# Performance work log

Hardware: AMD Instinct MI355X
Metric: run time of the kernel (lower is better)

The kernel has to match this reference:

```python
import jax, jax.numpy as jnp
import numpy as np

HIDDEN = 1024
INTER = 4096
NUM_EXPERTS = 8
TOP_K = 2


def setup_inputs() -> dict:
    key = jax.random.key(0)
    k1, k2, k3, k4 = jax.random.split(key, 4)
    hidden_states = jax.random.normal(k1, (4, 1024, HIDDEN), dtype=jnp.float32)
    gate_w = jax.random.normal(k2, (HIDDEN, NUM_EXPERTS), dtype=jnp.float32) * 0.02
    w1 = jax.random.normal(k3, (NUM_EXPERTS, HIDDEN, INTER), dtype=jnp.float32) * 0.02
    w2 = jax.random.normal(k4, (NUM_EXPERTS, INTER, HIDDEN), dtype=jnp.float32) * 0.02
    return {"hidden_states": hidden_states, "gate_w": gate_w, "w1": w1, "w2": w2}


def reference(hidden_states, gate_w, w1, w2):
    B, S, H = hidden_states.shape
    x = hidden_states.reshape(-1, H)                       # [T, H]
    T = x.shape[0]
    router_logits = x @ gate_w                             # [T, E]
    probs = jax.nn.softmax(router_logits.astype(jnp.float32), axis=-1)
    routing_weights, selected_experts = jax.lax.top_k(probs, TOP_K)  # [T, K]
    routing_weights = routing_weights / routing_weights.sum(-1, keepdims=True)
    routing_weights = routing_weights.astype(x.dtype)
    # combine[t, e] = sum_k rw[t, k] * (sel[t, k] == e)
    combine = jnp.zeros((T, NUM_EXPERTS), x.dtype).at[
        jnp.arange(T)[:, None], selected_experts
    ].add(routing_weights)
    # dense grouped MLP over all experts; zero combine weight drops unrouted pairs
    h1 = jax.nn.gelu(jnp.einsum('th,ehi->tei', x, w1), approximate=False)  # [T, E, I]
    y = jnp.einsum('tei,eih->teh', h1, w2)                 # [T, E, H]
    out = jnp.einsum('teh,te->th', y, combine)             # [T, H]
    return out.reshape(B, S, H), router_logits
```

## Files before the change

### kernel.cpp

```cpp
#include <hip/hip_runtime.h>
#include <hip/hip_bf16.h>
#include <math.h>

typedef unsigned short u16;
typedef unsigned int u32;
typedef __bf16 bf16x8 __attribute__((ext_vector_type(8)));
typedef float f32x4 __attribute__((ext_vector_type(4)));

#define T_TOK 4096
#define HID   1024
#define INTER 4096
#define NEXP  8

#define WS_NEEDED 209978368ull

__device__ __forceinline__ u16 f2bf(float f) {
    u32 u = __builtin_bit_cast(u32, f);
    u += 0x7FFFu + ((u >> 16) & 1u);
    return (u16)(u >> 16);
}

__device__ __forceinline__ void gl2lds16(const void* g, void* l) {
    __builtin_amdgcn_global_load_lds(
        (const __attribute__((address_space(1))) u32*)g,
        (__attribute__((address_space(3))) u32*)l, 16, 0, 0);
}

__device__ __forceinline__ float fast_gelu(float v) {
    float u2 = v * (-1.5957691216f - 0.0713548163f * v * v);
    return v / (1.0f + __expf(u2));
}

__global__ __launch_bounds__(256) void router_kernel(
    const float* __restrict__ x, const float* __restrict__ gw,
    float* __restrict__ logits, int* __restrict__ counts,
    int* __restrict__ tlist, float* __restrict__ wlist)
{
    const int lane = threadIdx.x & 63, wv = threadIdx.x >> 6;
    const int t = blockIdx.x * 4 + wv;
    const float* xr = x + (size_t)t * HID;
    float a[8] = {0.f,0.f,0.f,0.f,0.f,0.f,0.f,0.f};
    for (int h = lane; h < HID; h += 64) {
        float xv = xr[h];
        const float4* g4 = (const float4*)(gw + h * 8);
        float4 g0 = g4[0], g1 = g4[1];
        a[0] += xv * g0.x; a[1] += xv * g0.y; a[2] += xv * g0.z; a[3] += xv * g0.w;
        a[4] += xv * g1.x; a[5] += xv * g1.y; a[6] += xv * g1.z; a[7] += xv * g1.w;
    }
#pragma unroll
    for (int e = 0; e < 8; e++) {
        float v = a[e];
        for (int o = 32; o > 0; o >>= 1) v += __shfl_down(v, o, 64);
        a[e] = v;
    }
    if (lane == 0) {
#pragma unroll
        for (int e = 0; e < 8; e++) logits[(size_t)t * 8 + e] = a[e];
        int e1 = 0; float b1 = a[0];
        for (int e = 1; e < 8; e++) if (a[e] > b1) { b1 = a[e]; e1 = e; }
        int e2 = -1; float b2 = -1e30f;
        for (int e = 0; e < 8; e++) if (e != e1 && a[e] > b2) { b2 = a[e]; e2 = e; }
        float wa = 1.0f / (1.0f + expf(b2 - b1));
        float wb = 1.0f - wa;
        int p = atomicAdd(&counts[e1], 1);
        tlist[e1 * T_TOK + p] = t; wlist[e1 * T_TOK + p] = wa;
        p = atomicAdd(&counts[e2], 1);
        tlist[e2 * T_TOK + p] = t; wlist[e2 * T_TOK + p] = wb;
    }
}

__global__ void scan_kernel(const int* __restrict__ counts, int* __restrict__ offs)
{
    if (threadIdx.x == 0) {
        int s = 0;
        for (int e = 0; e < 8; e++) { offs[e] = s; s += counts[e]; }
    }
}

__global__ __launch_bounds__(256) void convert_x_kernel(
    const float* __restrict__ src, u16* __restrict__ dst)
{
    const int idx = (blockIdx.x * 256 + threadIdx.x) * 8;
    float4 f0 = *(const float4*)(src + idx);
    float4 f1 = *(const float4*)(src + idx + 4);
    uint4 o;
    o.x = (u32)f2bf(f0.x) | ((u32)f2bf(f0.y) << 16);
    o.y = (u32)f2bf(f0.z) | ((u32)f2bf(f0.w) << 16);
    o.z = (u32)f2bf(f1.x) | ((u32)f2bf(f1.y) << 16);
    o.w = (u32)f2bf(f1.z) | ((u32)f2bf(f1.w) << 16);
    *(uint4*)(dst + idx) = o;
}

__global__ __launch_bounds__(256) void transpose_convert_kernel(
    const float* __restrict__ src, u16* __restrict__ dst, int R, int C)
{
    __shared__ float tl[64][65];
    const int e = blockIdx.z;
    const int c0 = blockIdx.x * 64, r0 = blockIdx.y * 64;
    const float* s = src + (size_t)e * R * C + (size_t)r0 * C + c0;
    const int tid = threadIdx.x;
#pragma unroll
    for (int it = 0; it < 4; it++) {
        int idx = it * 256 + tid;
        int r = idx >> 4;
        int c4 = (idx & 15) * 4;
        float4 v = *(const float4*)(s + (size_t)r * C + c4);
        tl[c4 + 0][r] = v.x;
        tl[c4 + 1][r] = v.y;
        tl[c4 + 2][r] = v.z;
        tl[c4 + 3][r] = v.w;
    }
    __syncthreads();
    u16* d = dst + (size_t)e * C * R + (size_t)c0 * R + r0;
#pragma unroll
    for (int it = 0; it < 2; it++) {
        int idx = it * 256 + tid;
        int c = idx >> 3;
        int rg = (idx & 7) * 8;
        u32 o[4];
#pragma unroll
        for (int p = 0; p < 4; p++)
            o[p] = (u32)f2bf(tl[c][rg + 2 * p]) | ((u32)f2bf(tl[c][rg + 2 * p + 1]) << 16);
        *(uint4*)(d + (size_t)c * R + rg) = *(uint4*)o;
    }
}

__global__ __launch_bounds__(256, 1) void gemm1_kernel(
    const u16* __restrict__ xb, const u16* __restrict__ w1t,
    const int* __restrict__ counts, const int* __restrict__ offs,
    const int* __restrict__ tlist, u16* __restrict__ h1b)
{
    const int e = blockIdx.z, mt = blockIdx.y, nt = blockIdx.x;
    const int cnt = counts[e];
    if (mt * 128 >= cnt) return;
    __shared__ __align__(16) u16 As[8192];
    __shared__ __align__(16) u16 Bs[8192];
    __shared__ int toks[128];
    const int tid = threadIdx.x, lane = tid & 63, wv = tid >> 6;
    if (tid < 128) toks[tid] = tlist[e * T_TOK + min(mt * 128 + tid, cnt - 1)];
    __syncthreads();

    f32x4 acc[4][4] = {};
    const int wm = wv & 1, wn = wv >> 1;
    const int sj = tid >> 3, sp = tid & 7;

    size_t abase[4], bbase[4];
    const u16* w1base = w1t + ((size_t)e * INTER + (size_t)nt * 128) * HID;
#pragma unroll
    for (int j = 0; j < 4; j++) {
        int m = j * 32 + sj;
        abase[j] = (size_t)toks[m] * HID + ((sp - m) & 7) * 8;
        bbase[j] = (size_t)m * HID + ((sp - m) & 7) * 8;
    }

    for (int h0 = 0; h0 < HID; h0 += 64) {
#pragma unroll
        for (int j = 0; j < 4; j++)
            gl2lds16(xb + abase[j] + h0, &As[j * 2048 + wv * 512]);
#pragma unroll
        for (int j = 0; j < 4; j++)
            gl2lds16(w1base + bbase[j] + h0, &Bs[j * 2048 + wv * 512]);
        __syncthreads();
#pragma unroll
        for (int kk = 0; kk < 2; kk++) {
            bf16x8 a[4], b[4];
            const int jjb = kk * 4 + (lane >> 4);
#pragma unroll
            for (int i = 0; i < 4; i++) {
                int m = wm * 64 + i * 16 + (lane & 15);
                a[i] = *(const bf16x8*)&As[m * 64 + ((jjb + m) & 7) * 8];
            }
#pragma unroll
            for (int i = 0; i < 4; i++) {
                int n = wn * 64 + i * 16 + (lane & 15);
                b[i] = *(const bf16x8*)&Bs[n * 64 + ((jjb + n) & 7) * 8];
            }
#pragma unroll
            for (int i = 0; i < 4; i++)
#pragma unroll
                for (int j = 0; j < 4; j++)
                    acc[i][j] = __builtin_amdgcn_mfma_f32_16x16x32_bf16(
                        a[i], b[j], acc[i][j], 0, 0, 0);
        }
        __syncthreads();
    }

    const int pb = offs[e] + mt * 128;
    const bool full = (mt * 128 + 128 <= cnt);
#pragma unroll
    for (int i = 0; i < 4; i++) {
        const int mb = wm * 64 + i * 16 + ((lane >> 4) << 2);
#pragma unroll
        for (int j = 0; j < 4; j++) {
            const int n = nt * 128 + wn * 64 + j * 16 + (lane & 15);
#pragma unroll
            for (int r = 0; r < 4; r++) {
                const int m = mb + r;
                if (full || mt * 128 + m < cnt) {
                    h1b[(size_t)(pb + m) * INTER + n] = f2bf(fast_gelu(acc[i][j][r]));
                }
            }
        }
    }
}

__global__ __launch_bounds__(256, 1) void gemm2_kernel(
    const u16* __restrict__ h1b, const u16* __restrict__ w2t,
    const int* __restrict__ counts, const int* __restrict__ offs,
    const int* __restrict__ tlist, const float* __restrict__ wlist,
    float* __restrict__ out)
{
    const int e = blockIdx.z, mt = blockIdx.y;
    const int nt = blockIdx.x & 7, ks = blockIdx.x >> 3;
    const int cnt = counts[e];
    if (mt * 128 >= cnt) return;
    __shared__ __align__(16) u16 As[8192];
    __shared__ __align__(16) u16 Bs[8192];
    __shared__ int toks[128];
    __shared__ float wgt[128];
    const int tid = threadIdx.x, lane = tid & 63, wv = tid >> 6;
    if (tid < 128) {
        int gi = e * T_TOK + min(mt * 128 + tid, cnt - 1);
        toks[tid] = tlist[gi];
        wgt[tid] = wlist[gi];
    }
    __syncthreads();

    f32x4 acc[4][4] = {};
    const int wm = wv & 1, wn = wv >> 1;
    const int sj = tid >> 3, sp = tid & 7;

    size_t abase[4], bbase[4];
    const u16* w2base = w2t + ((size_t)e * HID + (size_t)nt * 128) * INTER;
    const int prow = offs[e];
#pragma unroll
    for (int j = 0; j < 4; j++) {
        int m = j * 32 + sj;
        int row = prow + min(mt * 128 + m, cnt - 1);
        abase[j] = (size_t)row * INTER + ((sp - m) & 7) * 8;
        bbase[j] = (size_t)m * INTER + ((sp - m) & 7) * 8;
    }

    const int i_lo = ks * (INTER / 2), i_hi = i_lo + (INTER / 2);
    for (int i0 = i_lo; i0 < i_hi; i0 += 64) {
#pragma unroll
        for (int j = 0; j < 4; j++)
            gl2lds16(h1b + abase[j] + i0, &As[j * 2048 + wv * 512]);
#pragma unroll
        for (int j = 0; j < 4; j++)
            gl2lds16(w2base + bbase[j] + i0, &Bs[j * 2048 + wv * 512]);
        __syncthreads();
#pragma unroll
        for (int kk = 0; kk < 2; kk++) {
            bf16x8 a[4], b[4];
            const int jjb = kk * 4 + (lane >> 4);
#pragma unroll
            for (int i = 0; i < 4; i++) {
                int m = wm * 64 + i * 16 + (lane & 15);
                a[i] = *(const bf16x8*)&As[m * 64 + ((jjb + m) & 7) * 8];
            }
#pragma unroll
            for (int i = 0; i < 4; i++) {
                int n = wn * 64 + i * 16 + (lane & 15);
                b[i] = *(const bf16x8*)&Bs[n * 64 + ((jjb + n) & 7) * 8];
            }
#pragma unroll
            for (int i = 0; i < 4; i++)
#pragma unroll
                for (int j = 0; j < 4; j++)
                    acc[i][j] = __builtin_amdgcn_mfma_f32_16x16x32_bf16(
                        a[i], b[j], acc[i][j], 0, 0, 0);
        }
        __syncthreads();
    }

    const bool full = (mt * 128 + 128 <= cnt);
#pragma unroll
    for (int i = 0; i < 4; i++) {
        const int mb = wm * 64 + i * 16 + ((lane >> 4) << 2);
#pragma unroll
        for (int j = 0; j < 4; j++) {
            const int n = nt * 128 + wn * 64 + j * 16 + (lane & 15);
#pragma unroll
            for (int r = 0; r < 4; r++) {
                const int m = mb + r;
                if (full || mt * 128 + m < cnt) {
                    atomicAdd(&out[(size_t)toks[m] * HID + n], acc[i][j][r] * wgt[m]);
                }
            }
        }
    }
}

extern "C" void kernel_launch(void* const* d_in, const int* in_sizes, int n_in,
                              void* d_out, int out_size, void* d_ws, size_t ws_size,
                              hipStream_t stream)
{
    const float* x  = (const float*)d_in[0];
    const float* gw = (const float*)d_in[1];
    const float* w1 = (const float*)d_in[2];
    const float* w2 = (const float*)d_in[3];
    float* out    = (float*)d_out;
    float* logits = out + 4194304;

    char* ws = (char*)d_ws;
    int*   counts = (int*)ws;
    int*   offs   = (int*)(ws + 256);
    int*   tlist  = (int*)(ws + 1024);
    float* wlist  = (float*)(ws + 132096);
    u16*   xb     = (u16*)(ws + 263168);
    u16*   w1t    = (u16*)(ws + 8651776);
    u16*   w2t    = (u16*)(ws + 75760640);
    u16*   h1b    = (u16*)(ws + 142869504);

    if (ws_size < WS_NEEDED) return;

    hipMemsetAsync(out, 0, 4194304 * sizeof(float), stream);
    hipMemsetAsync(counts, 0, 256, stream);

    router_kernel<<<1024, 256, 0, stream>>>(x, gw, logits, counts, tlist, wlist);
    scan_kernel<<<1, 64, 0, stream>>>(counts, offs);
    convert_x_kernel<<<2048, 256, 0, stream>>>(x, xb);
    transpose_convert_kernel<<<dim3(64, 16, 8), 256, 0, stream>>>(w1, w1t, HID, INTER);
    transpose_convert_kernel<<<dim3(16, 64, 8), 256, 0, stream>>>(w2, w2t, INTER, HID);

    gemm1_kernel<<<dim3(32, 16, 8), 256, 0, stream>>>(xb, w1t, counts, offs, tlist, h1b);
    gemm2_kernel<<<dim3(16, 16, 8), 256, 0, stream>>>(h1b, w2t, counts, offs, tlist, wlist, out);
}
```

Measured before the change: 707.5 us.

## Enlarge GEMM M-tile to 256, remap blocks per XCD, allow two blocks per CU

New measurement: 714.4 us. No clear change (+1.0%).

```diff
diff --git a/kernel.cpp b/kernel.cpp
--- a/kernel.cpp
+++ b/kernel.cpp
@@ -11,6 +11,10 @@
 #define HID   1024
 #define INTER 4096
 #define NEXP  8
+
+#define BM 256
+#define BN 128
+#define BK 64
 
 #define WS_NEEDED 209978368ull
 
@@ -125,37 +129,45 @@
     }
 }
 
-__global__ __launch_bounds__(256, 1) void gemm1_kernel(
+__global__ __launch_bounds__(256, 2) void gemm1_kernel(
     const u16* __restrict__ xb, const u16* __restrict__ w1t,
     const int* __restrict__ counts, const int* __restrict__ offs,
     const int* __restrict__ tlist, u16* __restrict__ h1b)
 {
-    const int e = blockIdx.z, mt = blockIdx.y, nt = blockIdx.x;
+    const int g = blockIdx.x & 7, p = blockIdx.x >> 3;
+    const int w = g * 256 + p;
+    const int e = w >> 8;
+    const int nt = (w >> 3) & 31;
+    const int mt = w & 7;
     const int cnt = counts[e];
-    if (mt * 128 >= cnt) return;
-    __shared__ __align__(16) u16 As[8192];
-    __shared__ __align__(16) u16 Bs[8192];
-    __shared__ int toks[128];
+    if (mt * BM >= cnt) return;
+    __shared__ __align__(16) u16 As[BM * BK];
+    __shared__ __align__(16) u16 Bs[BN * BK];
+    __shared__ int toks[BM];
     const int tid = threadIdx.x, lane = tid & 63, wv = tid >> 6;
-    if (tid < 128) toks[tid] = tlist[e * T_TOK + min(mt * 128 + tid, cnt - 1)];
+    toks[tid] = tlist[e * T_TOK + min(mt * BM + tid, cnt - 1)];
     __syncthreads();
 
-    f32x4 acc[4][4] = {};
+    f32x4 acc[8][4] = {};
     const int wm = wv & 1, wn = wv >> 1;
     const int sj = tid >> 3, sp = tid & 7;
 
-    size_t abase[4], bbase[4];
-    const u16* w1base = w1t + ((size_t)e * INTER + (size_t)nt * 128) * HID;
+    size_t abase[8], bbase[4];
+    const u16* w1base = w1t + ((size_t)e * INTER + (size_t)nt * BN) * HID;
+#pragma unroll
+    for (int j = 0; j < 8; j++) {
+        int m = j * 32 + sj;
+        abase[j] = (size_t)toks[m] * HID + ((sp - m) & 7) * 8;
+    }
 #pragma unroll
     for (int j = 0; j < 4; j++) {
         int m = j * 32 + sj;
-        abase[j] = (size_t)toks[m] * HID + ((sp - m) & 7) * 8;
         bbase[j] = (size_t)m * HID + ((sp - m) & 7) * 8;
     }
 
-    for (int h0 = 0; h0 < HID; h0 += 64) {
-#pragma unroll
-        for (int j = 0; j < 4; j++)
+    for (int h0 = 0; h0 < HID; h0 += BK) {
+#pragma unroll
+        for (int j = 0; j < 8; j++)
             gl2lds16(xb + abase[j] + h0, &As[j * 2048 + wv * 512]);
 #pragma unroll
         for (int j = 0; j < 4; j++)
@@ -163,20 +175,20 @@
         __syncthreads();
 #pragma unroll
         for (int kk = 0; kk < 2; kk++) {
-            bf16x8 a[4], b[4];
+            bf16x8 a[8], b[4];
             const int jjb = kk * 4 + (lane >> 4);
 #pragma unroll
-            for (int i = 0; i < 4; i++) {
-                int m = wm * 64 + i * 16 + (lane & 15);
+            for (int i = 0; i < 8; i++) {
+                int m = wm * 128 + i * 16 + (lane & 15);
                 a[i] = *(const bf16x8*)&As[m * 64 + ((jjb + m) & 7) * 8];
             }
 #pragma unroll
-            for (int i = 0; i < 4; i++) {
-                int n = wn * 64 + i * 16 + (lane & 15);
-                b[i] = *(const bf16x8*)&Bs[n * 64 + ((jjb + n) & 7) * 8];
-            }
-#pragma unroll
-            for (int i = 0; i < 4; i++)
+            for (int j = 0; j < 4; j++) {
+                int n = wn * 64 + j * 16 + (lane & 15);
+                b[j] = *(const bf16x8*)&Bs[n * 64 + ((jjb + n) & 7) * 8];
+            }
+#pragma unroll
+            for (int i = 0; i < 8; i++)
 #pragma unroll
                 for (int j = 0; j < 4; j++)
                     acc[i][j] = __builtin_amdgcn_mfma_f32_16x16x32_bf16(
@@ -185,66 +197,73 @@
         __syncthreads();
     }
 
-    const int pb = offs[e] + mt * 128;
-    const bool full = (mt * 128 + 128 <= cnt);
-#pragma unroll
-    for (int i = 0; i < 4; i++) {
-        const int mb = wm * 64 + i * 16 + ((lane >> 4) << 2);
+    const int pb = offs[e] + mt * BM;
+    const bool full = (mt * BM + BM <= cnt);
+#pragma unroll
+    for (int i = 0; i < 8; i++) {
+        const int mb = wm * 128 + i * 16 + ((lane >> 4) << 2);
 #pragma unroll
         for (int j = 0; j < 4; j++) {
-            const int n = nt * 128 + wn * 64 + j * 16 + (lane & 15);
+            const int n = nt * BN + wn * 64 + j * 16 + (lane & 15);
 #pragma unroll
             for (int r = 0; r < 4; r++) {
                 const int m = mb + r;
-                if (full || mt * 128 + m < cnt) {
+                if (full || mt * BM + m < cnt)
                     h1b[(size_t)(pb + m) * INTER + n] = f2bf(fast_gelu(acc[i][j][r]));
-                }
             }
         }
     }
 }
 
-__global__ __launch_bounds__(256, 1) void gemm2_kernel(
+__global__ __launch_bounds__(256, 2) void gemm2_kernel(
     const u16* __restrict__ h1b, const u16* __restrict__ w2t,
     const int* __restrict__ counts, const int* __restrict__ offs,
     const int* __restrict__ tlist, const float* __restrict__ wlist,
     float* __restrict__ out)
 {
-    const int e = blockIdx.z, mt = blockIdx.y;
-    const int nt = blockIdx.x & 7, ks = blockIdx.x >> 3;
+    const int g = blockIdx.x & 7, p = blockIdx.x >> 3;
+    const int w = g * 128 + p;
+    const int grp = w >> 6;
+    const int e = grp >> 1, ks = grp & 1;
+    const int nt = (w >> 3) & 7;
+    const int mt = w & 7;
     const int cnt = counts[e];
-    if (mt * 128 >= cnt) return;
-    __shared__ __align__(16) u16 As[8192];
-    __shared__ __align__(16) u16 Bs[8192];
-    __shared__ int toks[128];
-    __shared__ float wgt[128];
+    if (mt * BM >= cnt) return;
+    __shared__ __align__(16) u16 As[BM * BK];
+    __shared__ __align__(16) u16 Bs[BN * BK];
+    __shared__ int toks[BM];
+    __shared__ float wgt[BM];
     const int tid = threadIdx.x, lane = tid & 63, wv = tid >> 6;
-    if (tid < 128) {
-        int gi = e * T_TOK + min(mt * 128 + tid, cnt - 1);
+    {
+        int gi = e * T_TOK + min(mt * BM + tid, cnt - 1);
         toks[tid] = tlist[gi];
         wgt[tid] = wlist[gi];
     }
     __syncthreads();
 
-    f32x4 acc[4][4] = {};
+    f32x4 acc[8][4] = {};
     const int wm = wv & 1, wn = wv >> 1;
     const int sj = tid >> 3, sp = tid & 7;
 
-    size_t abase[4], bbase[4];
-    const u16* w2base = w2t + ((size_t)e * HID + (size_t)nt * 128) * INTER;
+    size_t abase[8], bbase[4];
+    const u16* w2base = w2t + ((size_t)e * HID + (size_t)nt * BN) * INTER;
     const int prow = offs[e];
+#pragma unroll
+    for (int j = 0; j < 8; j++) {
+        int m = j * 32 + sj;
+        int row = prow + min(mt * BM + m, cnt - 1);
+        abase[j] = (size_t)row * INTER + ((sp - m) & 7) * 8;
+    }
 #pragma unroll
     for (int j = 0; j < 4; j++) {
         int m = j * 32 + sj;
-        int row = prow + min(mt * 128 + m, cnt - 1);
-        abase[j] = (size_t)row * INTER + ((sp - m) & 7) * 8;
         bbase[j] = (size_t)m * INTER + ((sp - m) & 7) * 8;
     }
 
     const int i_lo = ks * (INTER / 2), i_hi = i_lo + (INTER / 2);
-    for (int i0 = i_lo; i0 < i_hi; i0 += 64) {
-#pragma unroll
-        for (int j = 0; j < 4; j++)
+    for (int i0 = i_lo; i0 < i_hi; i0 += BK) {
+#pragma unroll
+        for (int j = 0; j < 8; j++)
             gl2lds16(h1b + abase[j] + i0, &As[j * 2048 + wv * 512]);
 #pragma unroll
         for (int j = 0; j < 4; j++)
@@ -252,20 +271,20 @@
         __syncthreads();
 #pragma unroll
         for (int kk = 0; kk < 2; kk++) {
-            bf16x8 a[4], b[4];
+            bf16x8 a[8], b[4];
             const int jjb = kk * 4 + (lane >> 4);
 #pragma unroll
-            for (int i = 0; i < 4; i++) {
-                int m = wm * 64 + i * 16 + (lane & 15);
+            for (int i = 0; i < 8; i++) {
+                int m = wm * 128 + i * 16 + (lane & 15);
                 a[i] = *(const bf16x8*)&As[m * 64 + ((jjb + m) & 7) * 8];
             }
 #pragma unroll
-            for (int i = 0; i < 4; i++) {
-                int n = wn * 64 + i * 16 + (lane & 15);
-                b[i] = *(const bf16x8*)&Bs[n * 64 + ((jjb + n) & 7) * 8];
-            }
-#pragma unroll
-            for (int i = 0; i < 4; i++)
+            for (int j = 0; j < 4; j++) {
+                int n = wn * 64 + j * 16 + (lane & 15);
+                b[j] = *(const bf16x8*)&Bs[n * 64 + ((jjb + n) & 7) * 8];
+            }
+#pragma unroll
+            for (int i = 0; i < 8; i++)
 #pragma unroll
                 for (int j = 0; j < 4; j++)
                     acc[i][j] = __builtin_amdgcn_mfma_f32_16x16x32_bf16(
@@ -274,19 +293,18 @@
         __syncthreads();
     }
 
-    const bool full = (mt * 128 + 128 <= cnt);
-#pragma unroll
-    for (int i = 0; i < 4; i++) {
-        const int mb = wm * 64 + i * 16 + ((lane >> 4) << 2);
+    const bool full = (mt * BM + BM <= cnt);
+#pragma unroll
+    for (int i = 0; i < 8; i++) {
+        const int mb = wm * 128 + i * 16 + ((lane >> 4) << 2);
 #pragma unroll
         for (int j = 0; j < 4; j++) {
-            const int n = nt * 128 + wn * 64 + j * 16 + (lane & 15);
+            const int n = nt * BN + wn * 64 + j * 16 + (lane & 15);
 #pragma unroll
             for (int r = 0; r < 4; r++) {
                 const int m = mb + r;
-                if (full || mt * 128 + m < cnt) {
+                if (full || mt * BM + m < cnt)
                     atomicAdd(&out[(size_t)toks[m] * HID + n], acc[i][j][r] * wgt[m]);
-                }
             }
         }
     }
@@ -324,6 +342,6 @@
     transpose_convert_kernel<<<dim3(64, 16, 8), 256, 0, stream>>>(w1, w1t, HID, INTER);
     transpose_convert_kernel<<<dim3(16, 64, 8), 256, 0, stream>>>(w2, w2t, INTER, HID);
 
-    gemm1_kernel<<<dim3(32, 16, 8), 256, 0, stream>>>(xb, w1t, counts, offs, tlist, h1b);
-    gemm2_kernel<<<dim3(16, 16, 8), 256, 0, stream>>>(h1b, w2t, counts, offs, tlist, wlist, out);
-}
+    gemm1_kernel<<<2048, 256, 0, stream>>>(xb, w1t, counts, offs, tlist, h1b);
+    gemm2_kernel<<<1024, 256, 0, stream>>>(h1b, w2t, counts, offs, tlist, wlist, out);
+}
```
